# Kernel tuning notes

Hardware: AMD Instinct MI355X
Metric: run time of the kernel (lower is better)

The kernel has to match this reference:

```python
import jax, jax.numpy as jnp
import numpy as np

B, S, C, H = 2, 2048, 2048, 16
Dh = C // H
ROPE_THETA = 10000.0


def _rope(t):
    # t: [B, S, H, Dh]; rotate-half RoPE over head_dim
    half = Dh // 2
    inv_freq = 1.0 / (ROPE_THETA ** (jnp.arange(0, half, dtype=jnp.float32) / half))
    ang = jnp.arange(S, dtype=jnp.float32)[:, None] * inv_freq[None, :]  # [S, half]
    cos = jnp.cos(ang)[None, :, None, :]  # [1,S,1,half]
    sin = jnp.sin(ang)[None, :, None, :]
    t1, t2 = t[..., :half], t[..., half:]
    return jnp.concatenate([t1 * cos - t2 * sin, t2 * cos + t1 * sin], axis=-1)


def setup_inputs() -> dict:
    key = jax.random.key(0)
    k1, k2, k3 = jax.random.split(key, 3)
    x = jax.random.normal(k1, (B, S, C), dtype=jnp.float32)
    Wqkv = jax.random.normal(k2, (C, 3 * C), dtype=jnp.float32) * (C ** -0.5)
    Wproj = jax.random.normal(k3, (C, C), dtype=jnp.float32) * (C ** -0.5)
    return {"x": x, "Wqkv": Wqkv, "Wproj": Wproj}


def reference(x, Wqkv, Wproj):
    batch, seq, hidden = x.shape
    qkv = x @ Wqkv  # [B,S,3C]
    # NOTE: torch code chunks as k, q, v (k first)
    k, q, v = jnp.split(qkv, 3, axis=-1)
    k = k.reshape(batch, seq, H, Dh)
    q = q.reshape(batch, seq, H, Dh)
    v = v.reshape(batch, seq, H, Dh)
    k = _rope(k)
    q = _rope(q)
    scale = Dh ** -0.5
    scores = jnp.einsum('bqhd,bkhd->bhqk', q, k) * scale  # [B,H,S,S]
    causal = jnp.tril(jnp.ones((seq, seq), dtype=bool))
    scores = jnp.where(causal[None, None], scores, jnp.finfo(scores.dtype).min)
    attn = jax.nn.softmax(scores, axis=-1)
    out = jnp.einsum('bhqk,bkhd->bqhd', attn, v).reshape(batch, seq, hidden)
    return out @ Wproj
```

## Files before the change

### kernel.cpp

```cpp
#include <hip/hip_runtime.h>
#include <hip/hip_bf16.h>

#define B_   2
#define S_   2048
#define C_   2048
#define H_   16
#define DH   128
#define C3   (3 * C_)

typedef __attribute__((ext_vector_type(8))) short short8;
typedef __attribute__((ext_vector_type(4))) float floatx4;

__device__ __forceinline__ void gload16(const void* g, void* l) {
  __builtin_amdgcn_global_load_lds(
      (const __attribute__((address_space(1))) unsigned int*)g,
      (__attribute__((address_space(3))) unsigned int*)l, 16, 0, 0);
}

__device__ __forceinline__ unsigned pk_bf16(float a, float b) {
  union { __hip_bfloat16 h; unsigned short u; } ua, ub;
  ua.h = __float2bfloat16(a); ub.h = __float2bfloat16(b);
  return (unsigned)ua.u | ((unsigned)ub.u << 16);
}

__global__ __launch_bounds__(256) void cast_bf16_kernel(
    const float* __restrict__ in, __hip_bfloat16* __restrict__ out, int n4) {
  int i = blockIdx.x * blockDim.x + threadIdx.x;
  if (i >= n4) return;
  float4 v = ((const float4*)in)[i];
  union { __hip_bfloat16 b[4]; uint2 u; } t;
  t.b[0] = __float2bfloat16(v.x);
  t.b[1] = __float2bfloat16(v.y);
  t.b[2] = __float2bfloat16(v.z);
  t.b[3] = __float2bfloat16(v.w);
  ((uint2*)out)[i] = t.u;
}

__global__ __launch_bounds__(256) void transpose_cast_kernel(
    const float* __restrict__ in, __hip_bfloat16* __restrict__ out, int R, int Cc) {
  __shared__ float tile[32][33];
  int c0 = blockIdx.x * 32, r0 = blockIdx.y * 32;
  int tx = threadIdx.x & 31, ty = threadIdx.x >> 5;
#pragma unroll
  for (int k = 0; k < 4; ++k)
    tile[ty + 8 * k][tx] = in[(size_t)(r0 + ty + 8 * k) * Cc + c0 + tx];
  __syncthreads();
#pragma unroll
  for (int k = 0; k < 4; ++k)
    out[(size_t)(c0 + ty + 8 * k) * R + r0 + tx] = __float2bfloat16(tile[tx][ty + 8 * k]);
}

#define S_VMCNT2 do { asm volatile("s_waitcnt vmcnt(2)" ::: "memory"); \
                      __builtin_amdgcn_sched_barrier(0); } while (0)
#define S_LGKM0  do { asm volatile("s_waitcnt lgkmcnt(0)" ::: "memory"); \
                      __builtin_amdgcn_sched_barrier(0); } while (0)
#define S_BAR    do { __builtin_amdgcn_s_barrier(); \
                      __builtin_amdgcn_sched_barrier(0); } while (0)


#define RD_A4(dst, buf, mh, sl)                                                          \
  do {                                                                                   \
    const __hip_bfloat16* base_ =                                                        \
        lds + (buf) * 28672 + (wm * 128 + (mh) * 64 + lr) * 64 + ((sl) ? sw1 : sw0);     \
    _Pragma("unroll") for (int i_ = 0; i_ < 4; ++i_)                                     \
        dst[i_] = *(const short8*)(base_ + i_ * 1024);                                   \
  } while (0)

#define RD_B3(dst, buf, sl)                                                              \
  do {                                                                                   \
    const __hip_bfloat16* base_ =                                                        \
        lds + (buf) * 28672 + 16384 + (wn * 48 + lr) * 64 + ((sl) ? sw1 : sw0);          \
    _Pragma("unroll") for (int j_ = 0; j_ < 3; ++j_)                                     \
        dst[j_] = *(const short8*)(base_ + j_ * 1024);                                   \
  } while (0)

#define MFG(afp, bfp, mh)                                                                \
  do {                                                                                   \
    __builtin_amdgcn_s_setprio(1);                                                       \
    _Pragma("unroll") for (int i_ = 0; i_ < 4; ++i_)                                     \
    _Pragma("unroll") for (int j_ = 0; j_ < 3; ++j_)                                     \
        acc[(mh) * 4 + i_][j_] = __builtin_amdgcn_mfma_f32_16x16x32_bf16(                \
            afp[i_], bfp[j_], acc[(mh) * 4 + i_][j_], 0, 0, 0);                          \
    __builtin_amdgcn_s_setprio(0);                                                       \
  } while (0)

__global__ __launch_bounds__(512, 2) void gemm1_kernel(
    const __hip_bfloat16* __restrict__ A, const __hip_bfloat16* __restrict__ Bt,
    __hip_bfloat16* __restrict__ Cp) {
  const int K = 2048;
  __shared__ __hip_bfloat16 lds[2 * 28672];
  const int tid = threadIdx.x;
  const int lane = tid & 63, wv = tid >> 6;
  const int wm = wv >> 2, wn = wv & 3;
  const int lr = lane & 15, lq = lane >> 4;
  const int m0 = blockIdx.y * 256, n0 = blockIdx.x * 192;
  const int sw0 = (lq ^ (lr & 7)) << 3;
  const int sw1 = sw0 ^ 32;

  const __hip_bfloat16* Abase = A + (size_t)m0 * K;
  const __hip_bfloat16* Bbase = Bt + (size_t)n0 * K;

  auto stA = [&](int buf, int half, int kk) {
#pragma unroll
    for (int pp = 0; pp < 2; ++pp) {
      int p = half * 2 + pp;
      int idx = p * 512 + tid;
      int row = idx >> 3;
      int lc = (idx & 7) ^ (row & 7);
      gload16(Abase + (size_t)row * K + kk + lc * 8,
              (char*)lds + buf * 57344 + p * 8192 + wv * 1024);
    }
  };
  auto stB2 = [&](int buf, int kk) {
#pragma unroll
    for (int p = 0; p < 2; ++p) {
      int idx = p * 512 + tid;
      int row = idx >> 3;
      int lc = (idx & 7) ^ (row & 7);
      gload16(Bbase + (size_t)row * K + kk + lc * 8,
              (char*)lds + buf * 57344 + 32768 + p * 8192 + wv * 1024);
    }
  };
  auto stB1 = [&](int buf, int kk) {
    int idx = 2 * 512 + tid;
    int row = idx >> 3;
    int lc = (idx & 7) ^ (row & 7);
    gload16(Bbase + (size_t)row * K + kk + lc * 8,
            (char*)lds + buf * 57344 + 49152 + wv * 1024);
  };

  floatx4 acc[8][3] = {};
  short8 afA[4], afB[4], afC[4], afD[4], bfA[3], bfB[3];

  stA(0, 0, 0); stA(0, 1, 0); stB2(0, 0); stB1(0, 0);
  stA(1, 0, 64);

#pragma unroll 1
  for (int it = 0; it < 16; ++it) {
    const int t = 2 * it;
    const int kk1 = (t + 1) * 64;
    const int kk2 = (t + 2 < 32) ? (t + 2) * 64 : 0;
    const int kk3 = (t + 3 < 32) ? (t + 3) * 64 : 0;

    S_VMCNT2;
    S_BAR;
    RD_A4(afA, 0, 0, 0); RD_B3(bfA, 0, 0);
    stA(1, 1, kk1);
    S_LGKM0;
    MFG(afA, bfA, 0);
    S_BAR;
    RD_A4(afB, 0, 1, 0); RD_A4(afC, 0, 0, 1);
    stB2(1, kk1);
    S_LGKM0;
    MFG(afB, bfA, 1);
    S_BAR;
    RD_B3(bfB, 0, 1); RD_A4(afD, 0, 1, 1);
    stB1(1, kk1);
    S_LGKM0;
    MFG(afC, bfB, 0);
    S_BAR;
    stA(0, 0, kk2);
    MFG(afD, bfB, 1);
    S_BAR;

    S_VMCNT2;
    S_BAR;
    RD_A4(afA, 1, 0, 0); RD_B3(bfA, 1, 0);
    stA(0, 1, kk2);
    S_LGKM0;
    MFG(afA, bfA, 0);
    S_BAR;
    RD_A4(afB, 1, 1, 0); RD_A4(afC, 1, 0, 1);
    stB2(0, kk2);
    S_LGKM0;
    MFG(afB, bfA, 1);
    S_BAR;
    RD_B3(bfB, 1, 1); RD_A4(afD, 1, 1, 1);
    stB1(0, kk2);
    S_LGKM0;
    MFG(afC, bfB, 0);
    S_BAR;
    stA(1, 0, kk3);
    MFG(afD, bfB, 1);
    S_BAR;
  }

  asm volatile("s_waitcnt vmcnt(0)" ::: "memory");
  __builtin_amdgcn_sched_barrier(0);

#pragma unroll
  for (int i = 0; i < 8; ++i)
#pragma unroll
    for (int j = 0; j < 3; ++j)
#pragma unroll
      for (int r = 0; r < 4; ++r) {
        int row = m0 + wm * 128 + i * 16 + lq * 4 + r;
        int col = n0 + wn * 48 + j * 16 + lr;
        Cp[(size_t)row * 6144 + col] = __float2bfloat16(acc[i][j][r]);
      }
}

#define S_VMCNT6 do { asm volatile("s_waitcnt vmcnt(6)" ::: "memory"); \
                      __builtin_amdgcn_sched_barrier(0); } while (0)

template <int NCOLS, bool OUT_F32>
__global__ __launch_bounds__(512, 2) void gemm_dp_kernel(
    const __hip_bfloat16* __restrict__ A, const __hip_bfloat16* __restrict__ Bt,
    void* __restrict__ Cp) {
  const int K = 2048, NT = 32;
  __shared__ __hip_bfloat16 lds[3 * 24576];
  const int tid = threadIdx.x;
  const int lane = tid & 63, wv = tid >> 6;
  const int wm = wv >> 1, wn = wv & 1;
  const int lr = lane & 15, lq = lane >> 4;
  const int m0 = blockIdx.y * 256, n0 = blockIdx.x * 128;
  const int sw0 = (lq ^ (lr & 7)) << 3;
  const int sw1 = sw0 ^ 32;

  auto stageA = [&](int bw, int p, int kk) {
    int idx = p * 512 + tid;
    int row = idx >> 3;
    int lc = (idx & 7) ^ (row & 7);
    gload16(A + (size_t)(m0 + row) * K + kk + lc * 8,
            (char*)lds + (size_t)bw * 49152 + (size_t)(p * 512 + wv * 64) * 16);
  };
  auto stageB = [&](int bw, int p, int kk) {
    int idx = p * 512 + tid;
    int row = idx >> 3;
    int lc = (idx & 7) ^ (row & 7);
    gload16(Bt + (size_t)(n0 + row) * K + kk + lc * 8,
            (char*)lds + (size_t)bw * 49152 + 32768 + (size_t)(p * 512 + wv * 64) * 16);
  };

#pragma unroll
  for (int p = 0; p < 4; ++p) stageA(0, p, 0);
#pragma unroll
  for (int p = 0; p < 2; ++p) stageB(0, p, 0);
#pragma unroll
  for (int p = 0; p < 4; ++p) stageA(1, p, 64);
#pragma unroll
  for (int p = 0; p < 2; ++p) stageB(1, p, 64);

  floatx4 acc[4][4] = {};
  int br = 0, bw = 2;

#pragma unroll 1
  for (int t = 0; t < NT; ++t) {
    const int kk2 = (t + 2 < NT) ? (t + 2) * 64 : 0;

    S_VMCNT6;
    S_BAR;

    const __hip_bfloat16* Ab = lds + br * 24576 + (wm * 64 + lr) * 64;
    const __hip_bfloat16* Bb = lds + br * 24576 + 16384 + (wn * 64 + lr) * 64;

    short8 af0[4], bf0[4];
#pragma unroll
    for (int i = 0; i < 4; ++i) af0[i] = *(const short8*)(Ab + i * 1024 + sw0);
#pragma unroll
    for (int j = 0; j < 4; ++j) bf0[j] = *(const short8*)(Bb + j * 1024 + sw0);
    stageA(bw, 0, kk2); stageA(bw, 1, kk2); stageB(bw, 0, kk2);
    S_LGKM0;
    __builtin_amdgcn_s_setprio(1);
#pragma unroll
    for (int i = 0; i < 4; ++i)
#pragma unroll
      for (int j = 0; j < 4; ++j)
        acc[i][j] = __builtin_amdgcn_mfma_f32_16x16x32_bf16(af0[i], bf0[j], acc[i][j], 0, 0, 0);
    __builtin_amdgcn_s_setprio(0);

    short8 af1[4], bf1[4];
#pragma unroll
    for (int i = 0; i < 4; ++i) af1[i] = *(const short8*)(Ab + i * 1024 + sw1);
#pragma unroll
    for (int j = 0; j < 4; ++j) bf1[j] = *(const short8*)(Bb + j * 1024 + sw1);
    stageA(bw, 2, kk2); stageA(bw, 3, kk2); stageB(bw, 1, kk2);
    S_LGKM0;
    __builtin_amdgcn_s_setprio(1);
#pragma unroll
    for (int i = 0; i < 4; ++i)
#pragma unroll
      for (int j = 0; j < 4; ++j)
        acc[i][j] = __builtin_amdgcn_mfma_f32_16x16x32_bf16(af1[i], bf1[j], acc[i][j], 0, 0, 0);
    __builtin_amdgcn_s_setprio(0);

    br = (br == 2) ? 0 : br + 1;
    bw = (bw == 2) ? 0 : bw + 1;
  }

  asm volatile("s_waitcnt vmcnt(0)" ::: "memory");
  __builtin_amdgcn_sched_barrier(0);

#pragma unroll
  for (int i = 0; i < 4; ++i)
#pragma unroll
    for (int j = 0; j < 4; ++j)
#pragma unroll
      for (int r = 0; r < 4; ++r) {
        int row = m0 + wm * 64 + i * 16 + lq * 4 + r;
        int col = n0 + wn * 64 + j * 16 + lr;
        if (OUT_F32)
          ((float*)Cp)[(size_t)row * NCOLS + col] = acc[i][j][r];
        else
          ((__hip_bfloat16*)Cp)[(size_t)row * NCOLS + col] = __float2bfloat16(acc[i][j][r]);
      }
}

__global__ __launch_bounds__(256) void rope_kernel(__hip_bfloat16* __restrict__ qkv) {
  int i = blockIdx.x * blockDim.x + threadIdx.x;
  int d = i & 63;
  int h = (i >> 6) & 15;
  int row = i >> 10;
  int s = row & (S_ - 1);
  float invf = exp2f((float)d * (-13.287712379549449f / 64.0f));
  float ang = (float)s * invf;
  float sn, c;
  __sincosf(ang, &sn, &c);
  size_t base = (size_t)row * C3 + h * DH + d;
  float k1 = __bfloat162float(qkv[base]);
  float k2 = __bfloat162float(qkv[base + 64]);
  qkv[base]      = __float2bfloat16(k1 * c - k2 * sn);
  qkv[base + 64] = __float2bfloat16(k2 * c + k1 * sn);
  const float scale = 0.08838834764831845f * 1.4426950408889634f;
  float q1 = __bfloat162float(qkv[base + C_]);
  float q2 = __bfloat162float(qkv[base + C_ + 64]);
  qkv[base + C_]      = __float2bfloat16((q1 * c - q2 * sn) * scale);
  qkv[base + C_ + 64] = __float2bfloat16((q2 * c + q1 * sn) * scale);
}

__global__ __launch_bounds__(256) void vtrans_kernel(
    const __hip_bfloat16* __restrict__ qkv, __hip_bfloat16* __restrict__ vt) {
  __shared__ short T[64 * 144];
  const int tid = threadIdx.x;
  const int t = blockIdx.x, bh = blockIdx.y;
  const int b = bh >> 4, h = bh & 15;
  const size_t brow = (size_t)b * S_;
#pragma unroll
  for (int p = 0; p < 4; ++p) {
    int idx = p * 256 + tid;
    int row = idx >> 4, c8 = idx & 15;
    *(short8*)(T + row * 144 + c8 * 8) =
        *(const short8*)(qkv + (brow + t * 64 + row) * C3 + 2 * C_ + h * DH + c8 * 8);
  }
  __syncthreads();
#pragma unroll
  for (int p = 0; p < 4; ++p) {
    int L = p * 256 + tid;
    int d = L & 127, cs = L >> 7;
    short8 v;
#pragma unroll
    for (int j = 0; j < 8; ++j) v[j] = T[(cs * 8 + j) * 144 + d];
    *(short8*)(vt + ((size_t)bh * 32 + t) * 8192 + (size_t)L * 8) = v;
  }
}

__global__ __launch_bounds__(256, 2) void attn_kernel(
    const __hip_bfloat16* __restrict__ qkv,
    const __hip_bfloat16* __restrict__ vt_tiles,
    __hip_bfloat16* __restrict__ outp) {
  __shared__ __hip_bfloat16 Ks[64 * 128];
  __shared__ __hip_bfloat16 Vt[64 * 128];
  __shared__ __hip_bfloat16 Ps[4 * 32 * 72];

  const int tid = threadIdx.x, lane = tid & 63, wv = tid >> 6;
  const int lr = lane & 15, lq = lane >> 4;
  const int qt = gridDim.x - 1 - blockIdx.x;
  const int bh = blockIdx.y;
  const int b = bh >> 4, h = bh & 15;
  const int q0 = qt * 128;
  const int q0w = q0 + wv * 32;
  const size_t brow = (size_t)b * S_;

  short8 qf[2][4];
#pragma unroll
  for (int rt = 0; rt < 2; ++rt)
#pragma unroll
    for (int ks = 0; ks < 4; ++ks)
      qf[rt][ks] = *(const short8*)(qkv + (brow + q0w + rt * 16 + lr) * C3 + C_ + h * DH + ks * 32 + lq * 8);

  floatx4 of[2][8] = {};
  float l_run[2] = {0.0f, 0.0f};

  const int wrow_last = q0w + 31;
  const int nkt = 2 * qt + 2;
  for (int kt = 0; kt < nkt; ++kt) {
    const int kb = kt * 64;
#pragma unroll
    for (int p = 0; p < 4; ++p) {
      int L = p * 256 + wv * 64 + lane;
      int srow = L >> 4;
      int ck = (L & 15) ^ (srow & 15);
      gload16(qkv + (brow + kb + srow) * C3 + h * DH + ck * 8,
              (char*)Ks + (size_t)(p * 256 + wv * 64) * 16);
      gload16(vt_tiles + ((size_t)bh * 32 + kt) * 8192 + (size_t)L * 8,
              (char*)Vt + (size_t)(p * 256 + wv * 64) * 16);
    }
    __syncthreads();

    if (kb <= wrow_last) {
      floatx4 st[2][4] = {};
#pragma unroll
      for (int ks = 0; ks < 4; ++ks) {
        short8 kfr[4];
#pragma unroll
        for (int t4 = 0; t4 < 4; ++t4)
          kfr[t4] = *(const short8*)(Ks + ((t4 * 16 + lr) * 16 + ((ks * 4 + lq) ^ lr)) * 8);
#pragma unroll
        for (int rt = 0; rt < 2; ++rt)
#pragma unroll
          for (int t4 = 0; t4 < 4; ++t4)
            st[rt][t4] = __builtin_amdgcn_mfma_f32_16x16x32_bf16(kfr[t4], qf[rt][ks], st[rt][t4], 0, 0, 0);
      }

      if (kb + 63 > q0w) {
#pragma unroll
        for (int rt = 0; rt < 2; ++rt)
#pragma unroll
          for (int t4 = 0; t4 < 4; ++t4)
#pragma unroll
            for (int r = 0; r < 4; ++r) {
              int s = kb + t4 * 16 + lq * 4 + r;
              if (s > q0w + rt * 16 + lr) st[rt][t4][r] = -1e30f;
            }
      }

#pragma unroll
      for (int rt = 0; rt < 2; ++rt) {
        float rs = 0.0f;
#pragma unroll
        for (int t4 = 0; t4 < 4; ++t4)
#pragma unroll
          for (int r = 0; r < 4; ++r) {
            float pv = exp2f(st[rt][t4][r]);
            st[rt][t4][r] = pv;
            rs += pv;
          }
        rs += __shfl_xor(rs, 16);
        rs += __shfl_xor(rs, 32);
        l_run[rt] += rs;
      }

#pragma unroll
      for (int rt = 0; rt < 2; ++rt)
#pragma unroll
        for (int t4 = 0; t4 < 4; ++t4) {
          unsigned* pdst = (unsigned*)(Ps + (wv * 32 + rt * 16 + lr) * 72 + t4 * 16 + lq * 4);
          pdst[0] = pk_bf16(st[rt][t4][0], st[rt][t4][1]);
          pdst[1] = pk_bf16(st[rt][t4][2], st[rt][t4][3]);
        }

#pragma unroll
      for (int ks = 0; ks < 2; ++ks) {
        short8 pa[2];
#pragma unroll
        for (int rt = 0; rt < 2; ++rt)
          pa[rt] = *(const short8*)(Ps + (wv * 32 + rt * 16 + lr) * 72 + ks * 32 + lq * 8);
#pragma unroll
        for (int dt = 0; dt < 8; ++dt) {
          short8 vb = *(const short8*)(Vt + ((ks * 4 + lq) * 128 + dt * 16 + lr) * 8);
#pragma unroll
          for (int rt = 0; rt < 2; ++rt)
            of[rt][dt] = __builtin_amdgcn_mfma_f32_16x16x32_bf16(pa[rt], vb, of[rt][dt], 0, 0, 0);
        }
      }
    }
    __syncthreads();
  }

#pragma unroll
  for (int rt = 0; rt < 2; ++rt) {
    float linv = 1.0f / l_run[rt];
    floatx4 lv;
#pragma unroll
    for (int r = 0; r < 4; ++r) lv[r] = __shfl(linv, lq * 4 + r);
#pragma unroll
    for (int dt = 0; dt < 8; ++dt)
#pragma unroll
      for (int r = 0; r < 4; ++r)
        outp[(brow + q0w + rt * 16 + lq * 4 + r) * C_ + h * DH + dt * 16 + lr] =
            __float2bfloat16(of[rt][dt][r] * lv[r]);
  }
}

extern "C" void kernel_launch(void* const* d_in, const int* in_sizes, int n_in,
                              void* d_out, int out_size, void* d_ws, size_t ws_size,
                              hipStream_t stream) {
  const float* x = (const float*)d_in[0];
  const float* Wqkv = (const float*)d_in[1];
  const float* Wproj = (const float*)d_in[2];

  __hip_bfloat16* xb = (__hip_bfloat16*)d_ws;
  __hip_bfloat16* WqkvT = xb + (size_t)4096 * 2048;
  __hip_bfloat16* qkvb = WqkvT + (size_t)6144 * 2048;
  __hip_bfloat16* WprojT = WqkvT;
  __hip_bfloat16* vt_tiles = WqkvT + (size_t)2048 * 2048;
  __hip_bfloat16* attnb = xb;

  cast_bf16_kernel<<<8192, 256, 0, stream>>>(x, xb, (4096 * 2048) / 4);
  transpose_cast_kernel<<<dim3(6144 / 32, 2048 / 32), 256, 0, stream>>>(Wqkv, WqkvT, 2048, 6144);

  gemm1_kernel<<<dim3(6144 / 192, 4096 / 256), 512, 0, stream>>>(xb, WqkvT, qkvb);

  rope_kernel<<<(B_ * S_ * H_ * 64) / 256, 256, 0, stream>>>(qkvb);

  vtrans_kernel<<<dim3(32, 32), 256, 0, stream>>>(qkvb, vt_tiles);

  transpose_cast_kernel<<<dim3(2048 / 32, 2048 / 32), 256, 0, stream>>>(Wproj, WprojT, 2048, 2048);

  attn_kernel<<<dim3(16, 32), 256, 0, stream>>>(qkvb, vt_tiles, attnb);

  gemm_dp_kernel<2048, true><<<dim3(2048 / 128, 4096 / 256), 512, 0, stream>>>(
      attnb, WprojT, (float*)d_out);
}
```

Baseline: 373.6 us.

## Merge preprocessing kernels, vectorize RoPE, and remap attention block order

Combines the x cast and Wqkv transpose into one launch, and the RoPE, V-transpose and Wproj transpose into a second launch, using block-index ranges to pick the role of each block. This removes several kernel launches and the gaps between them. RoPE now handles 8 elements per thread with 16-byte loads and stores instead of scalar bf16 accesses. The attention grid is remapped so that, in block order, all heavy causal query tiles of every head come first and the light tiles come after, which is meant to improve load balance across the grid. The cost is a heterogeneous grid in which blocks with different work share one launch.

Result: faster. 347.0 us (-7.1%).

```diff
diff --git a/kernel.cpp b/kernel.cpp
--- a/kernel.cpp
+++ b/kernel.cpp
@@ -23,24 +23,21 @@
   return (unsigned)ua.u | ((unsigned)ub.u << 16);
 }
 
-__global__ __launch_bounds__(256) void cast_bf16_kernel(
-    const float* __restrict__ in, __hip_bfloat16* __restrict__ out, int n4) {
-  int i = blockIdx.x * blockDim.x + threadIdx.x;
-  if (i >= n4) return;
-  float4 v = ((const float4*)in)[i];
-  union { __hip_bfloat16 b[4]; uint2 u; } t;
-  t.b[0] = __float2bfloat16(v.x);
-  t.b[1] = __float2bfloat16(v.y);
-  t.b[2] = __float2bfloat16(v.z);
-  t.b[3] = __float2bfloat16(v.w);
-  ((uint2*)out)[i] = t.u;
-}
-
-__global__ __launch_bounds__(256) void transpose_cast_kernel(
-    const float* __restrict__ in, __hip_bfloat16* __restrict__ out, int R, int Cc) {
-  __shared__ float tile[32][33];
-  int c0 = blockIdx.x * 32, r0 = blockIdx.y * 32;
-  int tx = threadIdx.x & 31, ty = threadIdx.x >> 5;
+__device__ __forceinline__ float bf2f(short u) {
+  union { unsigned u; float f; } t;
+  t.u = ((unsigned)(unsigned short)u) << 16;
+  return t.f;
+}
+__device__ __forceinline__ short f2bf(float f) {
+  union { __hip_bfloat16 h; short s; } t;
+  t.h = __float2bfloat16(f);
+  return t.s;
+}
+
+__device__ __forceinline__ void transpose_cast_dev(
+    const float* __restrict__ in, __hip_bfloat16* __restrict__ out,
+    int R, int Cc, int c0, int r0, int tid, float (*tile)[33]) {
+  int tx = tid & 31, ty = tid >> 5;
 #pragma unroll
   for (int k = 0; k < 4; ++k)
     tile[ty + 8 * k][tx] = in[(size_t)(r0 + ty + 8 * k) * Cc + c0 + tx];
@@ -48,6 +45,27 @@
 #pragma unroll
   for (int k = 0; k < 4; ++k)
     out[(size_t)(c0 + ty + 8 * k) * R + r0 + tx] = __float2bfloat16(tile[tx][ty + 8 * k]);
+}
+
+__global__ __launch_bounds__(256) void pre_kernel(
+    const float* __restrict__ x, __hip_bfloat16* __restrict__ xb,
+    const float* __restrict__ Wqkv, __hip_bfloat16* __restrict__ WqkvT) {
+  __shared__ float tile[32][33];
+  const int bid = blockIdx.x, tid = threadIdx.x;
+  if (bid < 8192) {
+    int i = bid * 256 + tid;
+    float4 v = ((const float4*)x)[i];
+    union { __hip_bfloat16 b[4]; uint2 u; } t;
+    t.b[0] = __float2bfloat16(v.x);
+    t.b[1] = __float2bfloat16(v.y);
+    t.b[2] = __float2bfloat16(v.z);
+    t.b[3] = __float2bfloat16(v.w);
+    ((uint2*)xb)[i] = t.u;
+  } else {
+    int tb = bid - 8192;
+    int bx = tb % 192, by = tb / 192;
+    transpose_cast_dev(Wqkv, WqkvT, 2048, 6144, bx * 32, by * 32, tid, tile);
+  }
 }
 
 #define S_VMCNT2 do { asm volatile("s_waitcnt vmcnt(2)" ::: "memory"); \
@@ -56,7 +74,6 @@
                       __builtin_amdgcn_sched_barrier(0); } while (0)
 #define S_BAR    do { __builtin_amdgcn_s_barrier(); \
                       __builtin_amdgcn_sched_barrier(0); } while (0)
-
 
 #define RD_A4(dst, buf, mh, sl)                                                          \
   do {                                                                                   \
@@ -142,8 +159,7 @@
     const int kk2 = (t + 2 < 32) ? (t + 2) * 64 : 0;
     const int kk3 = (t + 3 < 32) ? (t + 3) * 64 : 0;
 
-    S_VMCNT2;
-    S_BAR;
+    S_VMCNT2; S_BAR;
     RD_A4(afA, 0, 0, 0); RD_B3(bfA, 0, 0);
     stA(1, 1, kk1);
     S_LGKM0;
@@ -163,8 +179,7 @@
     MFG(afD, bfB, 1);
     S_BAR;
 
-    S_VMCNT2;
-    S_BAR;
+    S_VMCNT2; S_BAR;
     RD_A4(afA, 1, 0, 0); RD_B3(bfA, 1, 0);
     stA(0, 1, kk2);
     S_LGKM0;
@@ -306,51 +321,69 @@
       }
 }
 
-__global__ __launch_bounds__(256) void rope_kernel(__hip_bfloat16* __restrict__ qkv) {
-  int i = blockIdx.x * blockDim.x + threadIdx.x;
-  int d = i & 63;
-  int h = (i >> 6) & 15;
-  int row = i >> 10;
-  int s = row & (S_ - 1);
-  float invf = exp2f((float)d * (-13.287712379549449f / 64.0f));
-  float ang = (float)s * invf;
-  float sn, c;
-  __sincosf(ang, &sn, &c);
-  size_t base = (size_t)row * C3 + h * DH + d;
-  float k1 = __bfloat162float(qkv[base]);
-  float k2 = __bfloat162float(qkv[base + 64]);
-  qkv[base]      = __float2bfloat16(k1 * c - k2 * sn);
-  qkv[base + 64] = __float2bfloat16(k2 * c + k1 * sn);
-  const float scale = 0.08838834764831845f * 1.4426950408889634f;
-  float q1 = __bfloat162float(qkv[base + C_]);
-  float q2 = __bfloat162float(qkv[base + C_ + 64]);
-  qkv[base + C_]      = __float2bfloat16((q1 * c - q2 * sn) * scale);
-  qkv[base + C_ + 64] = __float2bfloat16((q2 * c + q1 * sn) * scale);
-}
-
-__global__ __launch_bounds__(256) void vtrans_kernel(
-    const __hip_bfloat16* __restrict__ qkv, __hip_bfloat16* __restrict__ vt) {
-  __shared__ short T[64 * 144];
-  const int tid = threadIdx.x;
-  const int t = blockIdx.x, bh = blockIdx.y;
-  const int b = bh >> 4, h = bh & 15;
-  const size_t brow = (size_t)b * S_;
-#pragma unroll
-  for (int p = 0; p < 4; ++p) {
-    int idx = p * 256 + tid;
-    int row = idx >> 4, c8 = idx & 15;
-    *(short8*)(T + row * 144 + c8 * 8) =
-        *(const short8*)(qkv + (brow + t * 64 + row) * C3 + 2 * C_ + h * DH + c8 * 8);
-  }
-  __syncthreads();
-#pragma unroll
-  for (int p = 0; p < 4; ++p) {
-    int L = p * 256 + tid;
-    int d = L & 127, cs = L >> 7;
-    short8 v;
-#pragma unroll
-    for (int j = 0; j < 8; ++j) v[j] = T[(cs * 8 + j) * 144 + d];
-    *(short8*)(vt + ((size_t)bh * 32 + t) * 8192 + (size_t)L * 8) = v;
+__global__ __launch_bounds__(256) void mid_kernel(
+    __hip_bfloat16* __restrict__ qkv, __hip_bfloat16* __restrict__ vt,
+    const float* __restrict__ Wproj, __hip_bfloat16* __restrict__ WprojT) {
+  __shared__ char smem[18432];
+  const int bid = blockIdx.x, tid = threadIdx.x;
+
+  if (bid < 2048) {
+    int i = bid * 256 + tid;
+    int d8 = (i & 7) << 3;
+    int h = (i >> 3) & 15;
+    int row = i >> 7;
+    int s = row & (S_ - 1);
+    size_t base = (size_t)row * C3 + h * DH + d8;
+    short8 k1 = *(const short8*)(qkv + base);
+    short8 k2 = *(const short8*)(qkv + base + 64);
+    short8 q1 = *(const short8*)(qkv + base + C_);
+    short8 q2 = *(const short8*)(qkv + base + C_ + 64);
+    short8 ko1, ko2, qo1, qo2;
+    const float scale = 0.08838834764831845f * 1.4426950408889634f;
+#pragma unroll
+    for (int j = 0; j < 8; ++j) {
+      float invf = exp2f((float)(d8 + j) * (-13.287712379549449f / 64.0f));
+      float ang = (float)s * invf;
+      float sn, c;
+      __sincosf(ang, &sn, &c);
+      float a = bf2f(k1[j]), b = bf2f(k2[j]);
+      ko1[j] = f2bf(a * c - b * sn);
+      ko2[j] = f2bf(b * c + a * sn);
+      a = bf2f(q1[j]); b = bf2f(q2[j]);
+      qo1[j] = f2bf((a * c - b * sn) * scale);
+      qo2[j] = f2bf((b * c + a * sn) * scale);
+    }
+    *(short8*)(qkv + base) = ko1;
+    *(short8*)(qkv + base + 64) = ko2;
+    *(short8*)(qkv + base + C_) = qo1;
+    *(short8*)(qkv + base + C_ + 64) = qo2;
+  } else if (bid < 3072) {
+    short* T = (short*)smem;
+    const int t = (bid - 2048) & 31, bh = (bid - 2048) >> 5;
+    const int b = bh >> 4, h = bh & 15;
+    const size_t brow = (size_t)b * S_;
+#pragma unroll
+    for (int p = 0; p < 4; ++p) {
+      int idx = p * 256 + tid;
+      int row = idx >> 4, c8 = idx & 15;
+      *(short8*)(T + row * 144 + c8 * 8) =
+          *(const short8*)(qkv + (brow + t * 64 + row) * C3 + 2 * C_ + h * DH + c8 * 8);
+    }
+    __syncthreads();
+#pragma unroll
+    for (int p = 0; p < 4; ++p) {
+      int L = p * 256 + tid;
+      int d = L & 127, cs = L >> 7;
+      short8 v;
+#pragma unroll
+      for (int j = 0; j < 8; ++j) v[j] = T[(cs * 8 + j) * 144 + d];
+      *(short8*)(vt + ((size_t)bh * 32 + t) * 8192 + (size_t)L * 8) = v;
+    }
+  } else {
+    int tb = bid - 3072;
+    int bx = tb & 63, by = tb >> 6;
+    transpose_cast_dev(Wproj, WprojT, 2048, 2048, bx * 32, by * 32, tid,
+                       (float(*)[33])smem);
   }
 }
 
@@ -364,8 +397,10 @@
 
   const int tid = threadIdx.x, lane = tid & 63, wv = tid >> 6;
   const int lr = lane & 15, lq = lane >> 4;
-  const int qt = gridDim.x - 1 - blockIdx.x;
-  const int bh = blockIdx.y;
+  const int n = blockIdx.y * 16 + blockIdx.x;
+  const int half = n >> 8, rr = n & 255;
+  const int bh = rr >> 3, p = rr & 7;
+  const int qt = half ? p : 15 - p;
   const int b = bh >> 4, h = bh & 15;
   const int q0 = qt * 128;
   const int q0w = q0 + wv * 32;
@@ -386,14 +421,14 @@
   for (int kt = 0; kt < nkt; ++kt) {
     const int kb = kt * 64;
 #pragma unroll
-    for (int p = 0; p < 4; ++p) {
-      int L = p * 256 + wv * 64 + lane;
+    for (int pp = 0; pp < 4; ++pp) {
+      int L = pp * 256 + wv * 64 + lane;
       int srow = L >> 4;
       int ck = (L & 15) ^ (srow & 15);
       gload16(qkv + (brow + kb + srow) * C3 + h * DH + ck * 8,
-              (char*)Ks + (size_t)(p * 256 + wv * 64) * 16);
+              (char*)Ks + (size_t)(pp * 256 + wv * 64) * 16);
       gload16(vt_tiles + ((size_t)bh * 32 + kt) * 8192 + (size_t)L * 8,
-              (char*)Vt + (size_t)(p * 256 + wv * 64) * 16);
+              (char*)Vt + (size_t)(pp * 256 + wv * 64) * 16);
     }
     __syncthreads();
 
@@ -496,16 +531,11 @@
   __hip_bfloat16* vt_tiles = WqkvT + (size_t)2048 * 2048;
   __hip_bfloat16* attnb = xb;
 
-  cast_bf16_kernel<<<8192, 256, 0, stream>>>(x, xb, (4096 * 2048) / 4);
-  transpose_cast_kernel<<<dim3(6144 / 32, 2048 / 32), 256, 0, stream>>>(Wqkv, WqkvT, 2048, 6144);
+  pre_kernel<<<8192 + 12288, 256, 0, stream>>>(x, xb, Wqkv, WqkvT);
 
   gemm1_kernel<<<dim3(6144 / 192, 4096 / 256), 512, 0, stream>>>(xb, WqkvT, qkvb);
 
-  rope_kernel<<<(B_ * S_ * H_ * 64) / 256, 256, 0, stream>>>(qkvb);
-
-  vtrans_kernel<<<dim3(32, 32), 256, 0, stream>>>(qkvb, vt_tiles);
-
-  transpose_cast_kernel<<<dim3(2048 / 32, 2048 / 32), 256, 0, stream>>>(Wproj, WprojT, 2048, 2048);
+  mid_kernel<<<2048 + 1024 + 4096, 256, 0, stream>>>(qkvb, vt_tiles, Wproj, WprojT);
 
   attn_kernel<<<dim3(16, 32), 256, 0, stream>>>(qkvb, vt_tiles, attnb);
 
```
